# Optimization experiments

Measured on AMD Instinct MI355X. Metric: run time of the kernel, lower is better.

## Reference

```python
import jax, jax.numpy as jnp
import numpy as np

B, N, D, H = 4, 2048, 1024, 16
HD = D // H


def setup_inputs() -> dict:
    key = jax.random.key(0)
    ks = jax.random.split(key, 9)
    s = 1.0 / np.sqrt(D)
    return {
        "x": jax.random.normal(ks[0], (B, N, D), jnp.float32),
        "Wq": jax.random.normal(ks[1], (D, D), jnp.float32) * s,
        "bq": jnp.zeros((D,), jnp.float32),
        "Wk": jax.random.normal(ks[2], (D, D), jnp.float32) * s,
        "bk": jnp.zeros((D,), jnp.float32),
        "Wv": jax.random.normal(ks[3], (D, D), jnp.float32) * s,
        "bv": jnp.zeros((D,), jnp.float32),
        "Wo": jax.random.normal(ks[4], (D, D), jnp.float32) * s,
        "bo": jnp.zeros((D,), jnp.float32),
    }


def reference(x, Wq, bq, Wk, bk, Wv, bv, Wo, bo):
    Bx, Nx, Dx = x.shape
    q = x @ Wq + bq  # [B,N,D]
    k = x @ Wk + bk
    v = x @ Wv + bv
    # split heads -> [B,H,N,hd]
    q = q.reshape(Bx, Nx, H, HD).transpose(0, 2, 1, 3)
    k = k.reshape(Bx, Nx, H, HD).transpose(0, 2, 1, 3)
    v = v.reshape(Bx, Nx, H, HD).transpose(0, 2, 1, 3)
    q = q / jnp.sqrt(jnp.asarray(HD, q.dtype))
    scores = jnp.einsum("bhqd,bhkd->bhqk", q, k)
    # causal mask: additive -1e9 strictly above diagonal (matches torch.triu diag=1)
    mask = jnp.triu(jnp.full((Nx, Nx), -1e9, dtype=scores.dtype), k=1)
    probs = jax.nn.softmax(scores + mask, axis=-1)
    out = jnp.einsum("bhqk,bhkd->bhqd", probs, v)  # [B,H,N,hd]
    out = out.transpose(0, 2, 1, 3).reshape(Bx, Nx, Dx)  # concat heads
    return out @ Wo + bo
```

## Files before the change

### kernel.cpp

```cpp
#include <hip/hip_runtime.h>
#include <hip/hip_bf16.h>


#define BB 4
#define NN 2048
#define DD 1024
#define HH 16
#define HD 64
#define MM (BB * NN)

typedef __bf16 bf16;
typedef __bf16 bf16x4 __attribute__((ext_vector_type(4)));
typedef __bf16 bf16x8 __attribute__((ext_vector_type(8)));
typedef float f32x4 __attribute__((ext_vector_type(4)));

__device__ __forceinline__ void async_copy16(bf16* lds, const bf16* g) {
    __builtin_amdgcn_global_load_lds(
        (const __attribute__((address_space(1))) void*)g,
        (__attribute__((address_space(3))) void*)lds, 16, 0, 0);
}

__global__ void convert_x(const float* __restrict__ x, bf16* __restrict__ xb) {
    int i = (blockIdx.x * 256 + threadIdx.x) * 4;
    float4 v = *(const float4*)&x[i];
    xb[i + 0] = (bf16)v.x;
    xb[i + 1] = (bf16)v.y;
    xb[i + 2] = (bf16)v.z;
    xb[i + 3] = (bf16)v.w;
}

__global__ void transpose_w4(const float* __restrict__ W0, const float* __restrict__ W1,
                             const float* __restrict__ W2, const float* __restrict__ W3,
                             bf16* __restrict__ Wt) {
    __shared__ float tile[32][33];
    const float* W = (blockIdx.z == 0) ? W0 : (blockIdx.z == 1) ? W1
                    : (blockIdx.z == 2) ? W2 : W3;
    bf16* out = Wt + (size_t)blockIdx.z * DD * DD;
    int tx = threadIdx.x, ty = threadIdx.y;
    int x0 = blockIdx.x * 32, y0 = blockIdx.y * 32;
#pragma unroll
    for (int i = 0; i < 32; i += 8)
        tile[ty + i][tx] = W[(size_t)(y0 + ty + i) * DD + x0 + tx];
    __syncthreads();
#pragma unroll
    for (int i = 0; i < 32; i += 8)
        out[(size_t)(x0 + ty + i) * DD + y0 + tx] = (bf16)tile[tx][ty + i];
}

template <int MODE>
__global__ __launch_bounds__(256) void gemm_bt(
    const bf16* __restrict__ A, const bf16* __restrict__ Wt,
    const float* __restrict__ b0, const float* __restrict__ b1,
    const float* __restrict__ b2, void* __restrict__ out0,
    void* __restrict__ out1, void* __restrict__ out2) {
    const int K = DD;
    __shared__ __align__(16) bf16 smem[MODE == 0 ? 128 * 136 : 128 * 64];
    bf16* As = smem;
    bf16* Bs = smem + 128 * 32;
    bf16* Cs = smem;

    int m0 = blockIdx.x * 128;
    int n0 = blockIdx.y * 128;

    const bf16* Wz;
    const float* bias;
    void* out;
    float scale = 1.0f;
    int z = 0;
    if (MODE == 0) {
        z = blockIdx.z;
        Wz = Wt + (size_t)z * DD * DD;
        bias = (z == 0) ? b0 : ((z == 1) ? b1 : b2);
        out = (z == 0) ? out0 : ((z == 1) ? out1 : out2);
        if (z == 0) scale = 0.125f * 1.44269504f;
    } else {
        Wz = Wt; bias = b0; out = out0;
    }

    int tid = threadIdx.x;
    int w = tid >> 6, lane = tid & 63;
    int wm = w >> 1, wn = w & 1;
    int quad = lane >> 4, l16 = lane & 15;

    f32x4 acc[4][4];
#pragma unroll
    for (int i = 0; i < 4; i++)
#pragma unroll
        for (int j = 0; j < 4; j++) acc[i][j] = (f32x4){0.f, 0.f, 0.f, 0.f};

    for (int k0 = 0; k0 < K; k0 += 32) {
        __syncthreads();
#pragma unroll
        for (int j = 0; j < 2; j++) {
            int c = j * 256 + w * 64 + lane;
            int row = c >> 2, kk = (c & 3) * 8;
            async_copy16(&As[c * 8], &A[(size_t)(m0 + row) * K + k0 + kk]);
            async_copy16(&Bs[c * 8], &Wz[(size_t)(n0 + row) * K + k0 + kk]);
        }
        __syncthreads();

        bf16x8 af[4], bfm[4];
#pragma unroll
        for (int i = 0; i < 4; i++) {
            af[i] = *(const bf16x8*)&As[(wm * 64 + i * 16 + l16) * 32 + quad * 8];
            bfm[i] = *(const bf16x8*)&Bs[(wn * 64 + i * 16 + l16) * 32 + quad * 8];
        }
#pragma unroll
        for (int i = 0; i < 4; i++)
#pragma unroll
            for (int j = 0; j < 4; j++)
                acc[i][j] = __builtin_amdgcn_mfma_f32_16x16x32_bf16(
                    af[i], bfm[j], acc[i][j], 0, 0, 0);
    }

    if (MODE == 0) {
        __syncthreads();
#pragma unroll
        for (int j = 0; j < 4; j++) {
            int nl = wn * 64 + j * 16 + l16;
            float bv = bias[n0 + nl];
#pragma unroll
            for (int i = 0; i < 4; i++) {
#pragma unroll
                for (int r = 0; r < 4; r++) {
                    int ml = wm * 64 + i * 16 + quad * 4 + r;
                    bf16 v = (bf16)((acc[i][j][r] + bv) * scale);
                    if (z == 2) Cs[nl * 136 + ml] = v;
                    else        Cs[ml * 136 + nl] = v;
                }
            }
        }
        __syncthreads();

        int bidx = m0 >> 11;
        int tok0 = m0 & (NN - 1);
        int hh0 = n0 >> 6;
        if (z != 2) {
#pragma unroll
            for (int hf = 0; hf < 2; hf++) {
                bf16* base = (bf16*)out + ((size_t)(bidx * HH + hh0 + hf) * NN + tok0) * HD;
#pragma unroll
                for (int k = 0; k < 4; k++) {
                    int f = k * 2048 + tid * 8;
                    int tok = f >> 6, hd = f & 63;
                    *(bf16x8*)&base[f] = *(const bf16x8*)&Cs[tok * 136 + hf * 64 + hd];
                }
            }
        } else {
#pragma unroll
            for (int hf = 0; hf < 2; hf++) {
#pragma unroll
                for (int k = 0; k < 4; k++) {
                    int hd = k * 16 + (tid >> 4);
                    int tk = (tid & 15) * 8;
                    bf16* dst = (bf16*)out +
                        ((size_t)(bidx * HH + hh0 + hf) * HD + hd) * NN + tok0 + tk;
                    *(bf16x8*)dst = *(const bf16x8*)&Cs[(hf * 64 + hd) * 136 + tk];
                }
            }
        }
    } else {
#pragma unroll
        for (int j = 0; j < 4; j++) {
            int n = n0 + wn * 64 + j * 16 + l16;
            float bv = bias[n];
#pragma unroll
            for (int i = 0; i < 4; i++) {
                int mrow = m0 + wm * 64 + i * 16 + quad * 4;
#pragma unroll
                for (int r = 0; r < 4; r++)
                    ((float*)out)[(size_t)(mrow + r) * DD + n] = acc[i][j][r] + bv;
            }
        }
    }
}

__global__ __launch_bounds__(512, 4) void flash_attn(
    const bf16* __restrict__ Q, const bf16* __restrict__ Kg,
    const bf16* __restrict__ Vt_g, bf16* __restrict__ Oc) {
    __shared__ __align__(16) bf16 Ks[128 * 72];
    __shared__ __align__(16) bf16 Vs[64 * 136];

    int bh = blockIdx.x;
    int b = bh >> 4, h = bh & 15;
    int tid = threadIdx.x;
    int w = tid >> 6, lane = tid & 63;
    int quad = lane >> 4, l16 = lane & 15;

    const bf16* Qb = Q + (size_t)bh * NN * HD;
    const bf16* Kb = Kg + (size_t)bh * NN * HD;
    const bf16* Vtb = Vt_g + (size_t)bh * HD * NN;

    bf16x8 ones8;
#pragma unroll
    for (int i = 0; i < 8; i++) ones8[i] = (bf16)1.0f;

    int kr[2], kc[2], vd[2], vk[2];
#pragma unroll
    for (int j = 0; j < 2; j++) {
        int c = j * 512 + tid;
        kr[j] = c >> 3; kc[j] = (c & 7) * 8;
        vd[j] = c >> 4; vk[j] = (c & 15) * 8;
    }

    for (int phase = 0; phase < 2; phase++) {
        int qi = (phase == 0) ? blockIdx.y : (15 - blockIdx.y);
        int q0 = qi * 128;
        int qrow = q0 + w * 16 + l16;

        bf16x8 qf[2];
#pragma unroll
        for (int ks = 0; ks < 2; ks++)
            qf[ks] = *(const bf16x8*)&Qb[(size_t)qrow * HD + ks * 32 + quad * 8];

        f32x4 l_sum = (f32x4){0.f, 0.f, 0.f, 0.f};
        f32x4 o_acc[4];
#pragma unroll
        for (int di = 0; di < 4; di++) o_acc[di] = (f32x4){0.f, 0.f, 0.f, 0.f};

        bf16x8 kreg[2], vreg[2];
#pragma unroll
        for (int j = 0; j < 2; j++) {
            kreg[j] = *(const bf16x8*)&Kb[(size_t)kr[j] * HD + kc[j]];
            vreg[j] = *(const bf16x8*)&Vtb[(size_t)vd[j] * NN + vk[j]];
        }

        for (int t = 0; t <= qi; t++) {
            __syncthreads();
#pragma unroll
            for (int j = 0; j < 2; j++) {
                *(bf16x8*)&Ks[kr[j] * 72 + kc[j]] = kreg[j];
                *(bf16x8*)&Vs[vd[j] * 136 + vk[j]] = vreg[j];
            }
            __syncthreads();

            if (t < qi) {
                int kvn = (t + 1) * 128;
#pragma unroll
                for (int j = 0; j < 2; j++) {
                    kreg[j] = *(const bf16x8*)&Kb[(size_t)(kvn + kr[j]) * HD + kc[j]];
                    vreg[j] = *(const bf16x8*)&Vtb[(size_t)vd[j] * NN + kvn + vk[j]];
                }
            }

            int kv0 = t * 128;
            bool diag = (t == qi);
#pragma unroll
            for (int mi = 0; mi < 4; mi++) {
                int ba = 2 * mi, bb = 2 * mi + 1;
                bf16x8 ka0 = *(const bf16x8*)&Ks[(ba * 16 + l16) * 72 + quad * 8];
                bf16x8 ka1 = *(const bf16x8*)&Ks[(ba * 16 + l16) * 72 + 32 + quad * 8];
                bf16x8 kb0 = *(const bf16x8*)&Ks[(bb * 16 + l16) * 72 + quad * 8];
                bf16x8 kb1 = *(const bf16x8*)&Ks[(bb * 16 + l16) * 72 + 32 + quad * 8];
                f32x4 sa = (f32x4){0.f, 0.f, 0.f, 0.f};
                f32x4 sb = (f32x4){0.f, 0.f, 0.f, 0.f};
                sa = __builtin_amdgcn_mfma_f32_16x16x32_bf16(ka0, qf[0], sa, 0, 0, 0);
                sa = __builtin_amdgcn_mfma_f32_16x16x32_bf16(ka1, qf[1], sa, 0, 0, 0);
                sb = __builtin_amdgcn_mfma_f32_16x16x32_bf16(kb0, qf[0], sb, 0, 0, 0);
                sb = __builtin_amdgcn_mfma_f32_16x16x32_bf16(kb1, qf[1], sb, 0, 0, 0);
                bf16x4 pa4, pb4;
                if (diag) {
                    int kva = kv0 + ba * 16 + quad * 4;
                    int kvb = kv0 + bb * 16 + quad * 4;
#pragma unroll
                    for (int r = 0; r < 4; r++) {
                        pa4[r] = (bf16)((kva + r > qrow) ? 0.f : exp2f(sa[r]));
                        pb4[r] = (bf16)((kvb + r > qrow) ? 0.f : exp2f(sb[r]));
                    }
                } else {
#pragma unroll
                    for (int r = 0; r < 4; r++) {
                        pa4[r] = (bf16)exp2f(sa[r]);
                        pb4[r] = (bf16)exp2f(sb[r]);
                    }
                }
                bf16x8 pfrag = __builtin_shufflevector(pa4, pb4, 0, 1, 2, 3, 4, 5, 6, 7);
                l_sum = __builtin_amdgcn_mfma_f32_16x16x32_bf16(pfrag, ones8, l_sum, 0, 0, 0);
#pragma unroll
                for (int di = 0; di < 4; di++) {
                    const bf16* vrow = &Vs[(di * 16 + l16) * 136 + mi * 32 + quad * 4];
                    bf16x4 vlo = *(const bf16x4*)(vrow);
                    bf16x4 vhi = *(const bf16x4*)(vrow + 16);
                    bf16x8 vfrag = __builtin_shufflevector(vlo, vhi, 0, 1, 2, 3, 4, 5, 6, 7);
                    o_acc[di] = __builtin_amdgcn_mfma_f32_16x16x32_bf16(pfrag, vfrag, o_acc[di], 0, 0, 0);
                }
            }
        }

#pragma unroll
        for (int r = 0; r < 4; r++) {
            float inv = 1.0f / l_sum[r];
            int tok = q0 + w * 16 + quad * 4 + r;
#pragma unroll
            for (int di = 0; di < 4; di++) {
                int d = h * 64 + di * 16 + l16;
                Oc[((size_t)(b * NN + tok)) * DD + d] = (bf16)(o_acc[di][r] * inv);
            }
        }
    }
}

extern "C" void kernel_launch(void* const* d_in, const int* in_sizes, int n_in,
                              void* d_out, int out_size, void* d_ws, size_t ws_size,
                              hipStream_t stream) {
    const float* x  = (const float*)d_in[0];
    const float* Wq = (const float*)d_in[1];
    const float* bq = (const float*)d_in[2];
    const float* Wk = (const float*)d_in[3];
    const float* bk = (const float*)d_in[4];
    const float* Wv = (const float*)d_in[5];
    const float* bv = (const float*)d_in[6];
    const float* Wo = (const float*)d_in[7];
    const float* bo = (const float*)d_in[8];

    const size_t need = (size_t)(8388608ull * 5 + 4194304ull) * sizeof(bf16);
    if (ws_size < need) return;

    bf16* ws = (bf16*)d_ws;
    bf16* xb = ws;
    bf16* wt = xb + (size_t)MM * DD;
    bf16* Qw = wt + 4ull * DD * DD;
    bf16* Kw = Qw + (size_t)MM * DD;
    bf16* Vw = Kw + (size_t)MM * DD;
    bf16* Aw = Vw + (size_t)MM * DD;

    convert_x<<<dim3(MM * DD / 1024), 256, 0, stream>>>(x, xb);

    transpose_w4<<<dim3(32, 32, 4), dim3(32, 8), 0, stream>>>(Wq, Wk, Wv, Wo, wt);

    gemm_bt<0><<<dim3(MM / 128, DD / 128, 3), 256, 0, stream>>>(
        xb, wt, bq, bk, bv, Qw, Kw, Vw);

    flash_attn<<<dim3(BB * HH, 8), 512, 0, stream>>>(Qw, Kw, Vw, Aw);

    gemm_bt<1><<<dim3(MM / 128, DD / 128, 1), 256, 0, stream>>>(
        Aw, wt + 3ull * DD * DD, bo, bo, bo, d_out, d_out, d_out);
}
```

Measured before the change: 265.7 us.

## Double-buffer K/V tiles in LDS and pre-permute V^T layout for 16-byte fragment loads

The flash attention loop now keeps two LDS buffers for K and V. The next tile is written into the alternate buffer after compute, which cuts the per-iteration barriers from two to one. The QKV projection epilogue for V^T now permutes tokens within each 32-wide group, so the attention kernel can read a V fragment with one 16-byte LDS load instead of two 8-byte loads and a shuffle. This doubles LDS use per block, which may reduce occupancy under the 4-blocks launch bound.

```diff
diff --git a/kernel.cpp b/kernel.cpp
--- a/kernel.cpp
+++ b/kernel.cpp
@@ -152,10 +152,16 @@
 #pragma unroll
                 for (int k = 0; k < 4; k++) {
                     int hd = k * 16 + (tid >> 4);
-                    int tk = (tid & 15) * 8;
+                    int p0 = (tid & 15) * 8;
+                    int base32 = p0 & ~31;
+                    int qq = (p0 & 31) >> 3;
+                    const bf16* crow = &Cs[(hf * 64 + hd) * 136];
+                    bf16x4 lo = *(const bf16x4*)&crow[base32 + qq * 4];
+                    bf16x4 hi = *(const bf16x4*)&crow[base32 + qq * 4 + 16];
+                    bf16x8 v = __builtin_shufflevector(lo, hi, 0, 1, 2, 3, 4, 5, 6, 7);
                     bf16* dst = (bf16*)out +
-                        ((size_t)(bidx * HH + hh0 + hf) * HD + hd) * NN + tok0 + tk;
-                    *(bf16x8*)dst = *(const bf16x8*)&Cs[(hf * 64 + hd) * 136 + tk];
+                        ((size_t)(bidx * HH + hh0 + hf) * HD + hd) * NN + tok0 + p0;
+                    *(bf16x8*)dst = v;
                 }
             }
         }
@@ -178,8 +184,8 @@
 __global__ __launch_bounds__(512, 4) void flash_attn(
     const bf16* __restrict__ Q, const bf16* __restrict__ Kg,
     const bf16* __restrict__ Vt_g, bf16* __restrict__ Oc) {
-    __shared__ __align__(16) bf16 Ks[128 * 72];
-    __shared__ __align__(16) bf16 Vs[64 * 136];
+    __shared__ __align__(16) bf16 Ks[2][128 * 72];
+    __shared__ __align__(16) bf16 Vs[2][64 * 136];
 
     int bh = blockIdx.x;
     int b = bh >> 4, h = bh & 15;
@@ -224,16 +230,15 @@
             kreg[j] = *(const bf16x8*)&Kb[(size_t)kr[j] * HD + kc[j]];
             vreg[j] = *(const bf16x8*)&Vtb[(size_t)vd[j] * NN + vk[j]];
         }
+#pragma unroll
+        for (int j = 0; j < 2; j++) {
+            *(bf16x8*)&Ks[0][kr[j] * 72 + kc[j]] = kreg[j];
+            *(bf16x8*)&Vs[0][vd[j] * 136 + vk[j]] = vreg[j];
+        }
+        __syncthreads();
 
         for (int t = 0; t <= qi; t++) {
-            __syncthreads();
-#pragma unroll
-            for (int j = 0; j < 2; j++) {
-                *(bf16x8*)&Ks[kr[j] * 72 + kc[j]] = kreg[j];
-                *(bf16x8*)&Vs[vd[j] * 136 + vk[j]] = vreg[j];
-            }
-            __syncthreads();
-
+            int cur = t & 1;
             if (t < qi) {
                 int kvn = (t + 1) * 128;
 #pragma unroll
@@ -243,15 +248,17 @@
                 }
             }
 
+            const bf16* Kcur = Ks[cur];
+            const bf16* Vcur = Vs[cur];
             int kv0 = t * 128;
             bool diag = (t == qi);
 #pragma unroll
             for (int mi = 0; mi < 4; mi++) {
                 int ba = 2 * mi, bb = 2 * mi + 1;
-                bf16x8 ka0 = *(const bf16x8*)&Ks[(ba * 16 + l16) * 72 + quad * 8];
-                bf16x8 ka1 = *(const bf16x8*)&Ks[(ba * 16 + l16) * 72 + 32 + quad * 8];
-                bf16x8 kb0 = *(const bf16x8*)&Ks[(bb * 16 + l16) * 72 + quad * 8];
-                bf16x8 kb1 = *(const bf16x8*)&Ks[(bb * 16 + l16) * 72 + 32 + quad * 8];
+                bf16x8 ka0 = *(const bf16x8*)&Kcur[(ba * 16 + l16) * 72 + quad * 8];
+                bf16x8 ka1 = *(const bf16x8*)&Kcur[(ba * 16 + l16) * 72 + 32 + quad * 8];
+                bf16x8 kb0 = *(const bf16x8*)&Kcur[(bb * 16 + l16) * 72 + quad * 8];
+                bf16x8 kb1 = *(const bf16x8*)&Kcur[(bb * 16 + l16) * 72 + 32 + quad * 8];
                 f32x4 sa = (f32x4){0.f, 0.f, 0.f, 0.f};
                 f32x4 sb = (f32x4){0.f, 0.f, 0.f, 0.f};
                 sa = __builtin_amdgcn_mfma_f32_16x16x32_bf16(ka0, qf[0], sa, 0, 0, 0);
@@ -278,13 +285,21 @@
                 l_sum = __builtin_amdgcn_mfma_f32_16x16x32_bf16(pfrag, ones8, l_sum, 0, 0, 0);
 #pragma unroll
                 for (int di = 0; di < 4; di++) {
-                    const bf16* vrow = &Vs[(di * 16 + l16) * 136 + mi * 32 + quad * 4];
-                    bf16x4 vlo = *(const bf16x4*)(vrow);
-                    bf16x4 vhi = *(const bf16x4*)(vrow + 16);
-                    bf16x8 vfrag = __builtin_shufflevector(vlo, vhi, 0, 1, 2, 3, 4, 5, 6, 7);
+                    bf16x8 vfrag = *(const bf16x8*)&Vcur[(di * 16 + l16) * 136 + mi * 32 + quad * 8];
                     o_acc[di] = __builtin_amdgcn_mfma_f32_16x16x32_bf16(pfrag, vfrag, o_acc[di], 0, 0, 0);
                 }
             }
+
+            if (t < qi) {
+                bf16* Kn = Ks[cur ^ 1];
+                bf16* Vn = Vs[cur ^ 1];
+#pragma unroll
+                for (int j = 0; j < 2; j++) {
+                    *(bf16x8*)&Kn[kr[j] * 72 + kc[j]] = kreg[j];
+                    *(bf16x8*)&Vn[vd[j] * 136 + vk[j]] = vreg[j];
+                }
+            }
+            __syncthreads();
         }
 
 #pragma unroll
```

After: 251.6 us. 5.3% less time.
